# Kernel tuning notes

Measured on AMD Instinct MI355X. Metric: run time of the kernel, lower is better.

The kernel has to match this reference:

```python
import jax, jax.numpy as jnp
import numpy as np

B = 16384      # batch of numbers
D = 768        # embedding_dim
BINS = 10      # num_magnitude_bins
H = 8          # attention heads
HD = D // H


def _ln(x, g, b, eps=1e-5):
    m = jnp.mean(x, -1, keepdims=True)
    v = jnp.mean(jnp.square(x - m), -1, keepdims=True)
    return (x - m) / jnp.sqrt(v + eps) * g + b


def setup_inputs():
    key = jax.random.key(0)
    ks = jax.random.split(key, 10)
    w = lambda k, s: jax.random.normal(k, s, dtype=jnp.float32) * 0.02
    number = jax.random.normal(ks[0], (B, 1), dtype=jnp.float32) * 1e4
    bounds = np.concatenate([[-np.inf], -np.logspace(0, 15, BINS - 1), [0.0], np.logspace(0, 15, BINS - 1)])
    boundaries = jnp.asarray(np.unique(bounds), dtype=jnp.float32)
    d4 = D // 4
    return dict(
        number=number, boundaries=boundaries,
        mag_emb=jax.random.normal(ks[1], (2 * BINS, D), dtype=jnp.float32),
        se_w1=w(ks[2], (d4, 1)), se_b1=jnp.zeros(d4, jnp.float32),
        se_g1=jnp.ones(d4, jnp.float32), se_bt1=jnp.zeros(d4, jnp.float32),
        se_w2=w(ks[3], (D, d4)), se_b2=jnp.zeros(D, jnp.float32),
        ne_w=w(ks[4], (D, 2)), ne_b=jnp.zeros(D, jnp.float32),
        ne_g=jnp.ones(D, jnp.float32), ne_bt=jnp.zeros(D, jnp.float32),
        ce_w=w(ks[5], (D, 2)), ce_b=jnp.zeros(D, jnp.float32),
        ce_g=jnp.ones(D, jnp.float32), ce_bt=jnp.zeros(D, jnp.float32),
        in_proj_w=w(ks[6], (3 * D, D)), in_proj_b=jnp.zeros(3 * D, jnp.float32),
        out_proj_w=w(ks[7], (D, D)), out_proj_b=jnp.zeros(D, jnp.float32),
        magnitude_scale=jnp.ones(2 * BINS, jnp.float32),
        temperature=jnp.array(1.0, jnp.float32),
    )


def reference(number, boundaries, mag_emb, se_w1, se_b1, se_g1, se_bt1, se_w2, se_b2,
              ne_w, ne_b, ne_g, ne_bt, ce_w, ce_b, ce_g, ce_bt,
              in_proj_w, in_proj_b, out_proj_w, out_proj_b, magnitude_scale, temperature):
    signs = jnp.sign(number)
    abs_num = jnp.abs(number)
    log_abs = jnp.log1p(abs_num)
    scale_factor = jnp.floor(jnp.log10(abs_num + 1e-10))                      # [B,1]
    num_feat = jnp.concatenate([number / (jnp.max(abs_num) + 1e-10),
                                log_abs / (jnp.max(log_abs) + 1e-10)], -1)    # [B,2]
    ctx_feat = jnp.concatenate([signs, scale_factor / 16.0], -1)              # [B,2]
    num_enc = jax.nn.gelu(_ln(num_feat @ ne_w.T + ne_b, ne_g, ne_bt), approximate=False)
    ctx_enc = jax.nn.gelu(_ln(ctx_feat @ ce_w.T + ce_b, ce_g, ce_bt), approximate=False)
    # torch.bucketize(right=False) == searchsorted side='left'
    bin_idx = jnp.clip(jnp.searchsorted(boundaries, number[:, 0], side='left'), 0, 2 * BINS - 1)
    magnitude_emb = mag_emb[bin_idx]                                          # [B,D]
    h = jax.nn.gelu(_ln(scale_factor @ se_w1.T + se_b1, se_g1, se_bt1), approximate=False)
    scale_emb = h @ se_w2.T + se_b2                                           # [B,D]
    feats = jnp.stack([num_enc, magnitude_emb, scale_emb, ctx_enc], axis=1)   # [B,4,D]
    qkv = feats @ in_proj_w.T + in_proj_b                                     # [B,4,3D]
    q, k, v = jnp.split(qkv, 3, axis=-1)
    q = q.reshape(-1, 4, H, HD); k = k.reshape(-1, 4, H, HD); v = v.reshape(-1, 4, H, HD)
    att = jax.nn.softmax(jnp.einsum('bqhd,bkhd->bhqk', q, k) / jnp.sqrt(jnp.float32(HD)), axis=-1)
    ao = jnp.einsum('bhqk,bkhd->bqhd', att, v).reshape(-1, 4, D)
    ao = ao @ out_proj_w.T + out_proj_b                                       # [B,4,D]
    wts = jnp.array([0.4, 0.3, 0.2, 0.1], dtype=ao.dtype)
    out = jnp.sum(ao * wts[None, :, None], axis=1)                            # [B,D]
    sc = jax.nn.softplus(magnitude_scale[bin_idx] / temperature)[:, None]
    out = out * sc
    out = jnp.where(jnp.isnan(out), jnp.zeros_like(out), out)
    nrm = jnp.sqrt(jnp.sum(out * out, axis=-1, keepdims=True))
    return out / jnp.maximum(nrm, 1e-12)
```

## Files before the change

kernel.cpp:

```cpp
#include <hip/hip_runtime.h>
#include <hip/hip_bf16.h>
#include <math.h>

#define BB 16384
#define DD 768
#define NG 512
#define GR 1024
#define MROWS 1280
#define CPS 511
#define NCELL 1022
#define MIXR 2048

typedef __attribute__((ext_vector_type(8))) short bf16x8;
typedef __attribute__((ext_vector_type(4))) float f32x4;

__device__ short g_Abf[(size_t)MROWS * DD];
__device__ short g_W[(size_t)2304 * DD];
__device__ short g_WoutBf[(size_t)DD * DD];
__device__ short g_qkv[(size_t)MROWS * 2304];
__device__ short g_QKp[(size_t)16 * MROWS * 128];
__device__ short g_TabP[(size_t)16 * 128 * 128];
__device__ float g_scoref[(size_t)16 * MROWS * 128];
__device__ float g_sd[(size_t)MROWS * 8];
__device__ float g_tnode[GR];
__device__ int   g_creg[NCELL];
__device__ short g_mixedS[(size_t)MIXR * DD];
__device__ short g_preS[(size_t)MIXR * DD];
__device__ float g_maxabs;

__device__ inline unsigned short f2bf(float x) {
    union { float f; unsigned u; } v; v.f = x;
    unsigned r = v.u + 0x7fffu + ((v.u >> 16) & 1u);
    return (unsigned short)(r >> 16);
}
__device__ inline float bf2f(unsigned short h) {
    union { unsigned u; float f; } v; v.u = ((unsigned)h) << 16;
    return v.f;
}

__device__ inline float gelu_exact(float x) {
    return 0.5f * x * (1.0f + erff(x * 0.70710678118654752440f));
}

__device__ inline float block_sum256(float v, float* sbuf) {
    #pragma unroll
    for (int o = 32; o; o >>= 1) v += __shfl_xor(v, o);
    __syncthreads();
    if ((threadIdx.x & 63) == 0) sbuf[threadIdx.x >> 6] = v;
    __syncthreads();
    return sbuf[0] + sbuf[1] + sbuf[2] + sbuf[3];
}

__device__ inline int region_of(float x, const float* __restrict__ boundaries,
                                int* bin_o, int* sfi_o, int* si_o) {
    int bin = 0;
    #pragma unroll
    for (int j = 0; j < 20; ++j) bin += (boundaries[j] < x) ? 1 : 0;
    bin = min(bin, 19);
    float sf = floorf(log10f(fabsf(x) + 1e-10f));
    int sfi = min(max((int)sf + 10, 0), 15);
    int si = (x > 0.f) ? 2 : ((x < 0.f) ? 0 : 1);
    *bin_o = bin; *sfi_o = sfi; *si_o = si;
    return (bin << 6) | (sfi << 2) | si;
}

__global__ __launch_bounds__(1024) void k_absmax(const float* __restrict__ number) {
    const float4* n4 = reinterpret_cast<const float4*>(number);
    float v = 0.f;
    #pragma unroll
    for (int i = 0; i < 4; ++i) {
        float4 x = n4[threadIdx.x + 1024 * i];
        v = fmaxf(fmaxf(fabsf(x.x), fabsf(x.y)), fmaxf(fmaxf(fabsf(x.z), fabsf(x.w)), v));
    }
    #pragma unroll
    for (int o = 32; o; o >>= 1) v = fmaxf(v, __shfl_xor(v, o));
    __shared__ float sb[16];
    if ((threadIdx.x & 63) == 0) sb[threadIdx.x >> 6] = v;
    __syncthreads();
    if (threadIdx.x == 0) {
        float m = sb[0];
        #pragma unroll
        for (int i = 1; i < 16; ++i) m = fmaxf(m, sb[i]);
        g_maxabs = m;
    }
}

__global__ void k_tables(const float* __restrict__ mag_emb,
                         const float* __restrict__ se_w1, const float* __restrict__ se_b1,
                         const float* __restrict__ se_g1, const float* __restrict__ se_bt1,
                         const float* __restrict__ se_w2, const float* __restrict__ se_b2,
                         const float* __restrict__ ce_w, const float* __restrict__ ce_b,
                         const float* __restrict__ ce_g, const float* __restrict__ ce_bt,
                         const float* __restrict__ in_proj_w, const float* __restrict__ out_proj_w,
                         const float* __restrict__ ne_w, const float* __restrict__ ne_b,
                         const float* __restrict__ ne_g, const float* __restrict__ ne_bt) {
    __shared__ float sbuf[4];
    __shared__ float sh[192];
    const int t = threadIdx.x;
    const int blk = blockIdx.x;
    if (blk < 20) {
        #pragma unroll
        for (int i = 0; i < 3; ++i) {
            int d = t + 256 * i;
            g_Abf[(size_t)(GR + blk) * DD + d] = (short)f2bf(mag_emb[blk * DD + d]);
        }
    } else if (blk < 36) {
        int sfi = blk - 20;
        float sf = (float)(sfi - 10);
        float pre = 0.f;
        if (t < 192) pre = sf * se_w1[t] + se_b1[t];
        float s = block_sum256(t < 192 ? pre : 0.f, sbuf);
        float m = s / 192.f;
        float dd = (t < 192) ? (pre - m) : 0.f;
        float vv = block_sum256(dd * dd, sbuf);
        float inv = 1.f / sqrtf(vv / 192.f + 1e-5f);
        if (t < 192) sh[t] = gelu_exact((pre - m) * inv * se_g1[t] + se_bt1[t]);
        __syncthreads();
        #pragma unroll
        for (int i = 0; i < 3; ++i) {
            int d = t + 256 * i;
            float acc = se_b2[d];
            for (int j = 0; j < 192; ++j) acc += se_w2[d * 192 + j] * sh[j];
            g_Abf[(size_t)(GR + 20 + sfi) * DD + d] = (short)f2bf(acc);
        }
    } else if (blk < 84) {
        int c = blk - 36;
        int si = c >> 4, sfi = c & 15;
        float f0 = (float)(si - 1);
        float f1 = (float)(sfi - 10) / 16.f;
        float pre[3];
        float ps = 0.f;
        #pragma unroll
        for (int i = 0; i < 3; ++i) {
            int d = t + 256 * i;
            pre[i] = f0 * ce_w[2 * d] + f1 * ce_w[2 * d + 1] + ce_b[d];
            ps += pre[i];
        }
        float s = block_sum256(ps, sbuf);
        float m = s / 768.f;
        float qs = 0.f;
        #pragma unroll
        for (int i = 0; i < 3; ++i) { float dd = pre[i] - m; qs += dd * dd; }
        float vv = block_sum256(qs, sbuf);
        float inv = 1.f / sqrtf(vv / 768.f + 1e-5f);
        #pragma unroll
        for (int i = 0; i < 3; ++i) {
            int d = t + 256 * i;
            g_Abf[(size_t)(GR + 36 + c) * DD + d] =
                (short)f2bf(gelu_exact((pre[i] - m) * inv * ce_g[d] + ce_bt[d]));
        }
    } else if (blk < 256) {
        int row = GR + 84 + (blk - 84);
        #pragma unroll
        for (int i = 0; i < 3; ++i) g_Abf[(size_t)row * DD + t + 256 * i] = 0;
    } else if (blk < 2560) {
        int i = (blk - 256) * 256 + t;
        const bool second = (i >= 442368);
        const float* src = second ? out_proj_w : in_proj_w;
        short* dst = second ? g_WoutBf : g_W;
        int j = second ? (i - 442368) : i;
        const float4 v = *reinterpret_cast<const float4*>(&src[(size_t)j * 4]);
        ushort4 o;
        o.x = f2bf(v.x); o.y = f2bf(v.y); o.z = f2bf(v.z); o.w = f2bf(v.w);
        *reinterpret_cast<ushort4*>(&dst[(size_t)j * 4]) = o;
    } else {
        const int wid = t >> 6, lane = t & 63;
        const int r = (blk - 2560) * 4 + wid;
        const float mx = g_maxabs;
        const float L = log1pf(mx);
        const float dt = L / (float)(NG - 1);
        const int ri = r & (NG - 1);
        float tt = (float)ri * dt;
        if (ri > 0 && ri < NG - 1) {
            #pragma unroll
            for (int k = 0; k < 16; ++k) {
                float tb = log1pf(__expf((float)k * 2.302585093f));
                if (tb < L && (int)(tb / dt + 0.5f) == ri) tt = tb;
            }
            #pragma unroll
            for (int j = 0; j < 9; ++j) {
                float tb = log1pf(__expf((float)j * 1.875f * 2.302585093f));
                if (tb < L && (int)(tb / dt + 0.5f) == ri) tt = tb;
            }
        }
        if (lane == 0) g_tnode[r] = tt;
        const float ax = expm1f(tt);
        const float sgn = (r >= NG) ? -1.f : 1.f;
        const float a = sgn * ax / (mx + 1e-10f);
        const float b = tt / (L + 1e-10f);
        float pre[12];
        float s = 0.f;
        #pragma unroll
        for (int j = 0; j < 12; ++j) {
            int d = lane + 64 * j;
            float2 w = *reinterpret_cast<const float2*>(&ne_w[2 * d]);
            pre[j] = a * w.x + b * w.y + ne_b[d];
            s += pre[j];
        }
        #pragma unroll
        for (int o = 32; o; o >>= 1) s += __shfl_xor(s, o);
        float m = s / 768.f;
        float q = 0.f;
        #pragma unroll
        for (int j = 0; j < 12; ++j) { float dd = pre[j] - m; q += dd * dd; }
        #pragma unroll
        for (int o = 32; o; o >>= 1) q += __shfl_xor(q, o);
        float inv = 1.f / sqrtf(q / 768.f + 1e-5f);
        #pragma unroll
        for (int j = 0; j < 12; ++j) {
            int d = lane + 64 * j;
            g_Abf[(size_t)r * DD + d] = (short)f2bf(gelu_exact((pre[j] - m) * inv * ne_g[d] + ne_bt[d]));
        }
    }
}

__global__ __launch_bounds__(512, 4) void gemm_bt(int which, int N, int K) {
    const int z = blockIdx.z;
    const short* A = (which == 0) ? g_Abf : (which == 1) ? g_mixedS : g_QKp + (size_t)z * MROWS * 128;
    const short* B = (which == 0) ? g_W : (which == 2) ? g_TabP + (size_t)z * 128 * 128 : g_WoutBf;
    short* C = (which == 0) ? g_qkv : g_preS;
    float* Cf = g_scoref + (size_t)z * MROWS * 128;

    __shared__ short As[256 * 64];
    __shared__ short Bs[128 * 64];
    const int t = threadIdx.x;

    const int GX = gridDim.x;
    const int nwg = GX * gridDim.y;
    const int lin = blockIdx.y * GX + blockIdx.x;
    const int qq = nwg >> 3, rr = nwg & 7;
    const int xcd = lin & 7, idx = lin >> 3;
    const int nl = (xcd < rr ? xcd * (qq + 1) : rr * (qq + 1) + (xcd - rr) * qq) + idx;
    const int m0 = (nl / GX) * 256, n0 = (nl % GX) * 128;

    const int wid = t >> 6, lane = t & 63;
    const int wm = wid >> 1, wn = wid & 1;
    const int fr = lane & 15, ks = lane >> 4;

    f32x4 acc[4][4];
    #pragma unroll
    for (int m = 0; m < 4; ++m)
        #pragma unroll
        for (int n = 0; n < 4; ++n) acc[m][n] = (f32x4){0.f, 0.f, 0.f, 0.f};

    for (int k0 = 0; k0 < K; k0 += 64) {
        #pragma unroll
        for (int i = 0; i < 4; ++i) {
            int L = t + 512 * i;
            int row = L >> 3, sp = L & 7;
            int s = sp ^ (row & 7);
            const short* srcA = A + (size_t)(m0 + row) * K + k0 + s * 8;
            __builtin_amdgcn_global_load_lds(
                (const __attribute__((address_space(1))) unsigned int*)srcA,
                (__attribute__((address_space(3))) unsigned int*)((char*)As + L * 16), 16, 0, 0);
        }
        #pragma unroll
        for (int i = 0; i < 2; ++i) {
            int L = t + 512 * i;
            int row = L >> 3, sp = L & 7;
            int s = sp ^ (row & 7);
            const short* srcB = B + (size_t)(n0 + row) * K + k0 + s * 8;
            __builtin_amdgcn_global_load_lds(
                (const __attribute__((address_space(1))) unsigned int*)srcB,
                (__attribute__((address_space(3))) unsigned int*)((char*)Bs + L * 16), 16, 0, 0);
        }
        __syncthreads();
        #pragma unroll
        for (int kk = 0; kk < 2; ++kk) {
            bf16x8 af[4], bfr[4];
            #pragma unroll
            for (int m = 0; m < 4; ++m) {
                int row = wm * 64 + m * 16 + fr;
                int off = row * 128 + ((((kk << 2) | ks) ^ (row & 7)) * 16);
                af[m] = *(const bf16x8*)((const char*)As + off);
            }
            #pragma unroll
            for (int n = 0; n < 4; ++n) {
                int row = wn * 64 + n * 16 + fr;
                int off = row * 128 + ((((kk << 2) | ks) ^ (row & 7)) * 16);
                bfr[n] = *(const bf16x8*)((const char*)Bs + off);
            }
            #pragma unroll
            for (int m = 0; m < 4; ++m)
                #pragma unroll
                for (int n = 0; n < 4; ++n)
                    acc[m][n] = __builtin_amdgcn_mfma_f32_16x16x32_bf16(af[m], bfr[n], acc[m][n], 0, 0, 0);
        }
        __syncthreads();
    }

    #pragma unroll
    for (int m = 0; m < 4; ++m)
        #pragma unroll
        for (int n = 0; n < 4; ++n)
            #pragma unroll
            for (int j = 0; j < 4; ++j) {
                int row = m0 + wm * 64 + m * 16 + ks * 4 + j;
                int col = n0 + wn * 64 + n * 16 + fr;
                if (which == 2) Cf[(size_t)row * N + col] = acc[m][n][j];
                else C[(size_t)row * N + col] = (short)f2bf(acc[m][n][j]);
            }
}

__global__ void k_repack(const float* __restrict__ in_proj_b) {
    const int blk = blockIdx.x;
    if (blk < 1280) {
        const int idx = blk * 256 + threadIdx.x;
        const int z = idx / (MROWS * 16);
        const int rem = idx % (MROWS * 16);
        const int g = rem >> 4, c8 = rem & 15, d = c8 * 8;
        unsigned short o[8] = {0, 0, 0, 0, 0, 0, 0, 0};
        if (d < 96) {
            const int h = z & 7;
            const int off = (z < 8) ? 0 : 768;
            const float* bias = in_proj_b + off + h * 96 + d;
            const unsigned short* src = (const unsigned short*)g_qkv + (size_t)g * 2304 + off + h * 96 + d;
            #pragma unroll
            for (int c = 0; c < 8; ++c) o[c] = f2bf(bf2f(src[c]) + bias[c]);
        }
        *reinterpret_cast<bf16x8*>(g_QKp + (size_t)idx * 8) = *(const bf16x8*)o;
    } else if (blk < 1408) {
        const int i2 = (blk - 1280) * 256 + threadIdx.x;
        const int z = i2 / (128 * 16);
        const int rem = i2 % (128 * 16);
        const int j = rem >> 4, c8 = rem & 15, d = c8 * 8;
        unsigned short o[8] = {0, 0, 0, 0, 0, 0, 0, 0};
        if (d < 96 && j < 84) {
            const int h = z & 7;
            const int off = (z < 8) ? 768 : 0;
            const float* bias = in_proj_b + off + h * 96 + d;
            const unsigned short* src = (const unsigned short*)g_qkv + (size_t)(GR + j) * 2304 + off + h * 96 + d;
            #pragma unroll
            for (int c = 0; c < 8; ++c) o[c] = f2bf(bf2f(src[c]) + bias[c]);
        }
        *reinterpret_cast<bf16x8*>(g_TabP + (size_t)i2 * 8) = *(const bf16x8*)o;
    } else {
        const int wid = threadIdx.x >> 6, lane = threadIdx.x & 63;
        const int g = (blk - 1408) * 4 + wid;
        if (g >= GR + 84) return;
        const int h = lane >> 3, sub = lane & 7;
        const int d0 = h * 96 + sub * 12;
        const unsigned short* qrow = (const unsigned short*)g_qkv + (size_t)g * 2304 + d0;
        const unsigned short* krow = qrow + 768;
        const float* bq = in_proj_b + d0;
        const float* bk = in_proj_b + 768 + d0;
        float s = 0.f;
        #pragma unroll
        for (int c = 0; c < 12; ++c)
            s += (bf2f(qrow[c]) + bq[c]) * (bf2f(krow[c]) + bk[c]);
        s += __shfl_xor(s, 1);
        s += __shfl_xor(s, 2);
        s += __shfl_xor(s, 4);
        if (sub == 0) g_sd[(size_t)g * 8 + h] = s;
    }
}

__global__ void k_attn_cell(const float* __restrict__ boundaries,
                            const float* __restrict__ in_proj_b) {
    const int wid = threadIdx.x >> 6, lane = threadIdx.x & 63;
    const int mr = blockIdx.x * 4 + wid;
    if (mr >= 2 * NCELL) return;
    const int cid = mr >> 1, ep = mr & 1;
    const int s = cid / CPS, c = cid - s * CPS;
    const int node = s * NG + c + ep;
    const float tn0 = g_tnode[s * NG + c], tn1 = g_tnode[s * NG + c + 1];
    const float xmid = (s ? -1.f : 1.f) * expm1f(0.5f * (tn0 + tn1));
    int bin, sfi, si;
    const int re = region_of(xmid, boundaries, &bin, &sfi, &si);
    if (ep == 0 && lane == 0) g_creg[cid] = re;
    const int j3[3] = {bin, 20 + sfi, 36 + si * 16 + sfi};

    const int h = lane >> 3;
    const float isq = 0.1020620726159658f;
    float sc[4][4];
    sc[0][0] = g_sd[(size_t)node * 8 + h] * isq;
    const size_t su = ((size_t)h * MROWS + node) * 128;
    const size_t sw = ((size_t)(8 + h) * MROWS + node) * 128;
    #pragma unroll
    for (int jj = 0; jj < 3; ++jj) {
        sc[0][jj + 1] = g_scoref[su + j3[jj]] * isq;
        sc[jj + 1][0] = g_scoref[sw + j3[jj]] * isq;
    }
    #pragma unroll
    for (int ii = 0; ii < 3; ++ii)
        #pragma unroll
        for (int jj = 0; jj < 3; ++jj)
            sc[ii + 1][jj + 1] = g_scoref[((size_t)h * MROWS + GR + j3[ii]) * 128 + j3[jj]] * isq;

    const float wt[4] = {0.4f, 0.3f, 0.2f, 0.1f};
    float wtil[4] = {0.f, 0.f, 0.f, 0.f};
    #pragma unroll
    for (int i = 0; i < 4; ++i) {
        float mxs = fmaxf(fmaxf(sc[i][0], sc[i][1]), fmaxf(sc[i][2], sc[i][3]));
        float ex[4], den = 0.f;
        #pragma unroll
        for (int j = 0; j < 4; ++j) { ex[j] = __expf(sc[i][j] - mxs); den += ex[j]; }
        float idn = wt[i] / den;
        #pragma unroll
        for (int j = 0; j < 4; ++j) wtil[j] += ex[j] * idn;
    }

    const int d0 = lane * 12;
    float bv[12];
    #pragma unroll
    for (int c4 = 0; c4 < 3; ++c4) {
        float4 cc = *reinterpret_cast<const float4*>(&in_proj_b[1536 + d0 + c4 * 4]);
        bv[c4 * 4 + 0] = cc.x; bv[c4 * 4 + 1] = cc.y; bv[c4 * 4 + 2] = cc.z; bv[c4 * 4 + 3] = cc.w;
    }
    float mixv[12];
    {
        const unsigned short* r0 = (const unsigned short*)g_qkv + (size_t)node * 2304 + 1536 + d0;
        #pragma unroll
        for (int cc = 0; cc < 12; ++cc) mixv[cc] = wtil[0] * (bf2f(r0[cc]) + bv[cc]);
    }
    #pragma unroll
    for (int jj = 0; jj < 3; ++jj) {
        const unsigned short* rt = (const unsigned short*)g_qkv + (size_t)(GR + j3[jj]) * 2304 + 1536 + d0;
        const float w = wtil[jj + 1];
        #pragma unroll
        for (int cc = 0; cc < 12; ++cc) mixv[cc] += w * (bf2f(rt[cc]) + bv[cc]);
    }
    unsigned short ob[12];
    #pragma unroll
    for (int cc = 0; cc < 12; ++cc) ob[cc] = f2bf(mixv[cc]);
    unsigned short* mbase = (unsigned short*)g_mixedS + (size_t)mr * DD + d0;
    #pragma unroll
    for (int c4 = 0; c4 < 3; ++c4)
        *reinterpret_cast<ushort4*>(mbase + c4 * 4) =
            make_ushort4(ob[c4 * 4 + 0], ob[c4 * 4 + 1], ob[c4 * 4 + 2], ob[c4 * 4 + 3]);
}

__global__ void k_final(const float* __restrict__ number, const float* __restrict__ boundaries,
                        const float* __restrict__ in_proj_b, const float* __restrict__ out_proj_b,
                        float* __restrict__ out) {
    const int wid = threadIdx.x >> 6, lane = threadIdx.x & 63;
    const int e = blockIdx.x * 4 + wid;
    const float x = number[e];
    int bin, sfi, si;
    const int re = region_of(x, boundaries, &bin, &sfi, &si);

    const float mx = g_maxabs;
    const float L = log1pf(mx);
    const float dt = L / (float)(NG - 1);
    const float t = log1pf(fabsf(x));
    const int s = (x < 0.f) ? 1 : 0;
    const int base = s * NG;
    int i0 = min(max((int)(t / dt), 0), NG - 2);
    #pragma unroll
    for (int it = 0; it < 2; ++it) {
        if (i0 > 0 && t < g_tnode[base + i0]) --i0;
        else if (i0 < NG - 2 && t >= g_tnode[base + i0 + 1]) ++i0;
    }
    const float tn0 = g_tnode[base + i0], tn1 = g_tnode[base + i0 + 1];
    float w1 = (t - tn0) / (tn1 - tn0);
    w1 = fminf(fmaxf(w1, 0.f), 1.f);
    const float w0 = 1.f - w1;
    const int cid = s * CPS + i0;
    const int d0 = lane * 12;
    float o[12], ss = 0.f;

    if (g_creg[cid] == re) {
        const unsigned short* r0 = (const unsigned short*)g_preS + (size_t)(2 * cid) * DD + d0;
        const unsigned short* r1 = r0 + DD;
        #pragma unroll
        for (int c4 = 0; c4 < 3; ++c4) {
            float4 b = *reinterpret_cast<const float4*>(&out_proj_b[d0 + c4 * 4]);
            ushort4 u0 = *reinterpret_cast<const ushort4*>(r0 + c4 * 4);
            ushort4 u1 = *reinterpret_cast<const ushort4*>(r1 + c4 * 4);
            float p0 = w0 * bf2f(u0.x) + w1 * bf2f(u1.x) + b.x;
            float p1 = w0 * bf2f(u0.y) + w1 * bf2f(u1.y) + b.y;
            float p2 = w0 * bf2f(u0.z) + w1 * bf2f(u1.z) + b.z;
            float p3 = w0 * bf2f(u0.w) + w1 * bf2f(u1.w) + b.w;
            if (p0 != p0) p0 = 0.f;
            if (p1 != p1) p1 = 0.f;
            if (p2 != p2) p2 = 0.f;
            if (p3 != p3) p3 = 0.f;
            o[c4 * 4 + 0] = p0; o[c4 * 4 + 1] = p1; o[c4 * 4 + 2] = p2; o[c4 * 4 + 3] = p3;
            ss += p0 * p0 + p1 * p1 + p2 * p2 + p3 * p3;
        }
    } else {
        const int j3[3] = {bin, 20 + sfi, 36 + si * 16 + sfi};
        const int g0 = base + i0;
        const int h = lane >> 3;
        const float isq = 0.1020620726159658f;
        float sc[4][4];
        sc[0][0] = (w0 * g_sd[(size_t)g0 * 8 + h] + w1 * g_sd[(size_t)(g0 + 1) * 8 + h]) * isq;
        const size_t su0 = ((size_t)h * MROWS + g0) * 128;
        const size_t sw0 = ((size_t)(8 + h) * MROWS + g0) * 128;
        #pragma unroll
        for (int jj = 0; jj < 3; ++jj) {
            const int j = j3[jj];
            sc[0][jj + 1] = (w0 * g_scoref[su0 + j] + w1 * g_scoref[su0 + 128 + j]) * isq;
            sc[jj + 1][0] = (w0 * g_scoref[sw0 + j] + w1 * g_scoref[sw0 + 128 + j]) * isq;
        }
        #pragma unroll
        for (int ii = 0; ii < 3; ++ii)
            #pragma unroll
            for (int jj = 0; jj < 3; ++jj)
                sc[ii + 1][jj + 1] = g_scoref[((size_t)h * MROWS + GR + j3[ii]) * 128 + j3[jj]] * isq;
        const float wt[4] = {0.4f, 0.3f, 0.2f, 0.1f};
        float wtil[4] = {0.f, 0.f, 0.f, 0.f};
        #pragma unroll
        for (int i = 0; i < 4; ++i) {
            float mxs = fmaxf(fmaxf(sc[i][0], sc[i][1]), fmaxf(sc[i][2], sc[i][3]));
            float ex[4], den = 0.f;
            #pragma unroll
            for (int j = 0; j < 4; ++j) { ex[j] = __expf(sc[i][j] - mxs); den += ex[j]; }
            float idn = wt[i] / den;
            #pragma unroll
            for (int j = 0; j < 4; ++j) wtil[j] += ex[j] * idn;
        }
        float mixv[12];
        {
            const unsigned short* r0 = (const unsigned short*)g_qkv + (size_t)g0 * 2304 + 1536 + d0;
            const unsigned short* r1 = r0 + 2304;
            #pragma unroll
            for (int cc = 0; cc < 12; ++cc) {
                float bvv = in_proj_b[1536 + d0 + cc];
                mixv[cc] = wtil[0] * (w0 * bf2f(r0[cc]) + w1 * bf2f(r1[cc]) + bvv);
            }
        }
        #pragma unroll
        for (int jj = 0; jj < 3; ++jj) {
            const unsigned short* rt = (const unsigned short*)g_qkv + (size_t)(GR + j3[jj]) * 2304 + 1536 + d0;
            const float w = wtil[jj + 1];
            #pragma unroll
            for (int cc = 0; cc < 12; ++cc)
                mixv[cc] += w * (bf2f(rt[cc]) + in_proj_b[1536 + d0 + cc]);
        }
        int mb[12];
        #pragma unroll
        for (int cc = 0; cc < 12; ++cc) mb[cc] = (int)f2bf(mixv[cc]);
        float acc[12];
        #pragma unroll
        for (int cc = 0; cc < 12; ++cc) acc[cc] = 0.f;
        for (int l = 0; l < 64; ++l) {
            float md[12];
            #pragma unroll
            for (int cc = 0; cc < 12; ++cc)
                md[cc] = bf2f((unsigned short)__shfl(mb[cc], l));
            const int dbase = l * 12;
            #pragma unroll
            for (int c2 = 0; c2 < 12; ++c2) {
                const unsigned short* rp = (const unsigned short*)g_WoutBf + (size_t)(d0 + c2) * DD + dbase;
                float a = 0.f;
                #pragma unroll
                for (int cc = 0; cc < 12; ++cc) a += md[cc] * bf2f(rp[cc]);
                acc[c2] += a;
            }
        }
        #pragma unroll
        for (int cc = 0; cc < 12; ++cc) {
            float p = acc[cc] + out_proj_b[d0 + cc];
            if (p != p) p = 0.f;
            o[cc] = p;
            ss += p * p;
        }
    }

    #pragma unroll
    for (int ofs = 32; ofs; ofs >>= 1) ss += __shfl_xor(ss, ofs);
    float inv = 1.f / fmaxf(sqrtf(ss), 1e-12f);
    float* obase = &out[(size_t)e * DD + d0];
    #pragma unroll
    for (int c4 = 0; c4 < 3; ++c4)
        *reinterpret_cast<float4*>(obase + c4 * 4) =
            make_float4(o[c4 * 4 + 0] * inv, o[c4 * 4 + 1] * inv, o[c4 * 4 + 2] * inv, o[c4 * 4 + 3] * inv);
}

extern "C" void kernel_launch(void* const* d_in, const int* in_sizes, int n_in,
                              void* d_out, int out_size, void* d_ws, size_t ws_size,
                              hipStream_t stream) {
    const float* number      = (const float*)d_in[0];
    const float* boundaries  = (const float*)d_in[1];
    const float* mag_emb     = (const float*)d_in[2];
    const float* se_w1       = (const float*)d_in[3];
    const float* se_b1       = (const float*)d_in[4];
    const float* se_g1       = (const float*)d_in[5];
    const float* se_bt1      = (const float*)d_in[6];
    const float* se_w2       = (const float*)d_in[7];
    const float* se_b2       = (const float*)d_in[8];
    const float* ne_w        = (const float*)d_in[9];
    const float* ne_b        = (const float*)d_in[10];
    const float* ne_g        = (const float*)d_in[11];
    const float* ne_bt       = (const float*)d_in[12];
    const float* ce_w        = (const float*)d_in[13];
    const float* ce_b        = (const float*)d_in[14];
    const float* ce_g        = (const float*)d_in[15];
    const float* ce_bt       = (const float*)d_in[16];
    const float* in_proj_w   = (const float*)d_in[17];
    const float* in_proj_b   = (const float*)d_in[18];
    const float* out_proj_w  = (const float*)d_in[19];
    const float* out_proj_b  = (const float*)d_in[20];
    float* out = (float*)d_out;

    k_absmax<<<1, 1024, 0, stream>>>(number);
    k_tables<<<2816, 256, 0, stream>>>(mag_emb, se_w1, se_b1, se_g1, se_bt1, se_w2, se_b2,
                                       ce_w, ce_b, ce_g, ce_bt, in_proj_w, out_proj_w,
                                       ne_w, ne_b, ne_g, ne_bt);
    gemm_bt<<<dim3(2304 / 128, MROWS / 256, 1), 512, 0, stream>>>(0, 2304, DD);
    k_repack<<<1685, 256, 0, stream>>>(in_proj_b);
    gemm_bt<<<dim3(1, MROWS / 256, 16), 512, 0, stream>>>(2, 128, 128);
    k_attn_cell<<<(2 * NCELL + 3) / 4, 256, 0, stream>>>(boundaries, in_proj_b);
    gemm_bt<<<dim3(DD / 128, MIXR / 256, 1), 512, 0, stream>>>(1, DD, DD);
    k_final<<<BB / 4, 256, 0, stream>>>(number, boundaries, in_proj_b, out_proj_b, out);
}
```

Measured before the change: 119.3 us.

## Fold absmax and repack kernels into table build and GEMM epilogue

Removes the separate absmax kernel by having each grid-table block redundantly reduce the max of the input numbers. Removes the repack kernel by having the QKV GEMM epilogue add bias and scatter Q/K into the padded per-head layouts, with the zero padding now written by k_tables. The per-node q·k self-dot is recomputed inline in k_attn_cell and k_final rather than precomputed. This cuts two launches and one pass over the QKV buffer, at the cost of redundant reductions, scattered 2-byte stores in the GEMM epilogue, and extra global reads in k_final.

```diff
diff --git a/kernel.cpp b/kernel.cpp
--- a/kernel.cpp
+++ b/kernel.cpp
@@ -21,7 +21,6 @@
 __device__ short g_QKp[(size_t)16 * MROWS * 128];
 __device__ short g_TabP[(size_t)16 * 128 * 128];
 __device__ float g_scoref[(size_t)16 * MROWS * 128];
-__device__ float g_sd[(size_t)MROWS * 8];
 __device__ float g_tnode[GR];
 __device__ int   g_creg[NCELL];
 __device__ short g_mixedS[(size_t)MIXR * DD];
@@ -64,28 +63,8 @@
     return (bin << 6) | (sfi << 2) | si;
 }
 
-__global__ __launch_bounds__(1024) void k_absmax(const float* __restrict__ number) {
-    const float4* n4 = reinterpret_cast<const float4*>(number);
-    float v = 0.f;
-    #pragma unroll
-    for (int i = 0; i < 4; ++i) {
-        float4 x = n4[threadIdx.x + 1024 * i];
-        v = fmaxf(fmaxf(fabsf(x.x), fabsf(x.y)), fmaxf(fmaxf(fabsf(x.z), fabsf(x.w)), v));
-    }
-    #pragma unroll
-    for (int o = 32; o; o >>= 1) v = fmaxf(v, __shfl_xor(v, o));
-    __shared__ float sb[16];
-    if ((threadIdx.x & 63) == 0) sb[threadIdx.x >> 6] = v;
-    __syncthreads();
-    if (threadIdx.x == 0) {
-        float m = sb[0];
-        #pragma unroll
-        for (int i = 1; i < 16; ++i) m = fmaxf(m, sb[i]);
-        g_maxabs = m;
-    }
-}
-
-__global__ void k_tables(const float* __restrict__ mag_emb,
+__global__ void k_tables(const float* __restrict__ number,
+                         const float* __restrict__ mag_emb,
                          const float* __restrict__ se_w1, const float* __restrict__ se_b1,
                          const float* __restrict__ se_g1, const float* __restrict__ se_bt1,
                          const float* __restrict__ se_w2, const float* __restrict__ se_b2,
@@ -96,6 +75,7 @@
                          const float* __restrict__ ne_g, const float* __restrict__ ne_bt) {
     __shared__ float sbuf[4];
     __shared__ float sh[192];
+    __shared__ float smx[4];
     const int t = threadIdx.x;
     const int blk = blockIdx.x;
     if (blk < 20) {
@@ -163,10 +143,23 @@
         ushort4 o;
         o.x = f2bf(v.x); o.y = f2bf(v.y); o.z = f2bf(v.z); o.w = f2bf(v.w);
         *reinterpret_cast<ushort4*>(&dst[(size_t)j * 4]) = o;
-    } else {
+    } else if (blk < 2816) {
+        const float4* n4 = reinterpret_cast<const float4*>(number);
+        float vmx = 0.f;
+        #pragma unroll
+        for (int i = 0; i < 16; ++i) {
+            float4 xx = n4[t + 256 * i];
+            vmx = fmaxf(fmaxf(fabsf(xx.x), fabsf(xx.y)), fmaxf(fmaxf(fabsf(xx.z), fabsf(xx.w)), vmx));
+        }
+        #pragma unroll
+        for (int o = 32; o; o >>= 1) vmx = fmaxf(vmx, __shfl_xor(vmx, o));
+        if ((t & 63) == 0) smx[t >> 6] = vmx;
+        __syncthreads();
+        const float mx = fmaxf(fmaxf(smx[0], smx[1]), fmaxf(smx[2], smx[3]));
+        if (t == 0) g_maxabs = mx;
+
         const int wid = t >> 6, lane = t & 63;
         const int r = (blk - 2560) * 4 + wid;
-        const float mx = g_maxabs;
         const float L = log1pf(mx);
         const float dt = L / (float)(NG - 1);
         const int ri = r & (NG - 1);
@@ -211,10 +204,22 @@
             int d = lane + 64 * j;
             g_Abf[(size_t)r * DD + d] = (short)f2bf(gelu_exact((pre[j] - m) * inv * ne_g[d] + ne_bt[d]));
         }
-    }
-}
-
-__global__ __launch_bounds__(512, 4) void gemm_bt(int which, int N, int K) {
+    } else if (blk < 3136) {
+        const int i = (blk - 2816) * 256 + t;
+        const int z = i / (MROWS * 4);
+        const int rem = i % (MROWS * 4);
+        const int row = rem >> 2, c = rem & 3;
+        const bf16x8 zv = {0, 0, 0, 0, 0, 0, 0, 0};
+        *reinterpret_cast<bf16x8*>(g_QKp + ((size_t)z * MROWS + row) * 128 + 96 + c * 8) = zv;
+    } else {
+        const int i = (blk - 3136) * 256 + t;
+        const bf16x8 zv = {0, 0, 0, 0, 0, 0, 0, 0};
+        *reinterpret_cast<bf16x8*>(g_TabP + (size_t)i * 8) = zv;
+    }
+}
+
+__global__ __launch_bounds__(512, 4) void gemm_bt(int which, int N, int K,
+                                                  const float* __restrict__ bias) {
     const int z = blockIdx.z;
     const short* A = (which == 0) ? g_Abf : (which == 1) ? g_mixedS : g_QKp + (size_t)z * MROWS * 128;
     const short* B = (which == 0) ? g_W : (which == 2) ? g_TabP + (size_t)z * 128 * 128 : g_WoutBf;
@@ -297,62 +302,25 @@
             for (int j = 0; j < 4; ++j) {
                 int row = m0 + wm * 64 + m * 16 + ks * 4 + j;
                 int col = n0 + wn * 64 + n * 16 + fr;
-                if (which == 2) Cf[(size_t)row * N + col] = acc[m][n][j];
-                else C[(size_t)row * N + col] = (short)f2bf(acc[m][n][j]);
-            }
-}
-
-__global__ void k_repack(const float* __restrict__ in_proj_b) {
-    const int blk = blockIdx.x;
-    if (blk < 1280) {
-        const int idx = blk * 256 + threadIdx.x;
-        const int z = idx / (MROWS * 16);
-        const int rem = idx % (MROWS * 16);
-        const int g = rem >> 4, c8 = rem & 15, d = c8 * 8;
-        unsigned short o[8] = {0, 0, 0, 0, 0, 0, 0, 0};
-        if (d < 96) {
-            const int h = z & 7;
-            const int off = (z < 8) ? 0 : 768;
-            const float* bias = in_proj_b + off + h * 96 + d;
-            const unsigned short* src = (const unsigned short*)g_qkv + (size_t)g * 2304 + off + h * 96 + d;
-            #pragma unroll
-            for (int c = 0; c < 8; ++c) o[c] = f2bf(bf2f(src[c]) + bias[c]);
-        }
-        *reinterpret_cast<bf16x8*>(g_QKp + (size_t)idx * 8) = *(const bf16x8*)o;
-    } else if (blk < 1408) {
-        const int i2 = (blk - 1280) * 256 + threadIdx.x;
-        const int z = i2 / (128 * 16);
-        const int rem = i2 % (128 * 16);
-        const int j = rem >> 4, c8 = rem & 15, d = c8 * 8;
-        unsigned short o[8] = {0, 0, 0, 0, 0, 0, 0, 0};
-        if (d < 96 && j < 84) {
-            const int h = z & 7;
-            const int off = (z < 8) ? 768 : 0;
-            const float* bias = in_proj_b + off + h * 96 + d;
-            const unsigned short* src = (const unsigned short*)g_qkv + (size_t)(GR + j) * 2304 + off + h * 96 + d;
-            #pragma unroll
-            for (int c = 0; c < 8; ++c) o[c] = f2bf(bf2f(src[c]) + bias[c]);
-        }
-        *reinterpret_cast<bf16x8*>(g_TabP + (size_t)i2 * 8) = *(const bf16x8*)o;
-    } else {
-        const int wid = threadIdx.x >> 6, lane = threadIdx.x & 63;
-        const int g = (blk - 1408) * 4 + wid;
-        if (g >= GR + 84) return;
-        const int h = lane >> 3, sub = lane & 7;
-        const int d0 = h * 96 + sub * 12;
-        const unsigned short* qrow = (const unsigned short*)g_qkv + (size_t)g * 2304 + d0;
-        const unsigned short* krow = qrow + 768;
-        const float* bq = in_proj_b + d0;
-        const float* bk = in_proj_b + 768 + d0;
-        float s = 0.f;
-        #pragma unroll
-        for (int c = 0; c < 12; ++c)
-            s += (bf2f(qrow[c]) + bq[c]) * (bf2f(krow[c]) + bk[c]);
-        s += __shfl_xor(s, 1);
-        s += __shfl_xor(s, 2);
-        s += __shfl_xor(s, 4);
-        if (sub == 0) g_sd[(size_t)g * 8 + h] = s;
-    }
+                float av = acc[m][n][j];
+                if (which == 2) {
+                    Cf[(size_t)row * N + col] = av;
+                } else {
+                    C[(size_t)row * N + col] = (short)f2bf(av);
+                    if (which == 0 && col < 1536) {
+                        int colh = (col >= 768) ? col - 768 : col;
+                        int h = (colh * 683) >> 16;
+                        int d = colh - h * 96;
+                        int zq = (col >= 768) ? 8 + h : h;
+                        unsigned short vb = f2bf(av + bias[col]);
+                        g_QKp[((size_t)zq * MROWS + row) * 128 + d] = (short)vb;
+                        if (row >= GR && row < GR + 84) {
+                            int zt = (col >= 768) ? h : 8 + h;
+                            g_TabP[((size_t)zt * 128 + (row - GR)) * 128 + d] = (short)vb;
+                        }
+                    }
+                }
+            }
 }
 
 __global__ void k_attn_cell(const float* __restrict__ boundaries,
@@ -370,10 +338,24 @@
     if (ep == 0 && lane == 0) g_creg[cid] = re;
     const int j3[3] = {bin, 20 + sfi, 36 + si * 16 + sfi};
 
+    const int d0 = lane * 12;
     const int h = lane >> 3;
     const float isq = 0.1020620726159658f;
+
+    float sdv = 0.f;
+    {
+        const unsigned short* qn = (const unsigned short*)g_qkv + (size_t)node * 2304 + d0;
+        const unsigned short* kn = qn + 768;
+        #pragma unroll
+        for (int cc = 0; cc < 12; ++cc)
+            sdv += (bf2f(qn[cc]) + in_proj_b[d0 + cc]) * (bf2f(kn[cc]) + in_proj_b[768 + d0 + cc]);
+        sdv += __shfl_xor(sdv, 1);
+        sdv += __shfl_xor(sdv, 2);
+        sdv += __shfl_xor(sdv, 4);
+    }
+
     float sc[4][4];
-    sc[0][0] = g_sd[(size_t)node * 8 + h] * isq;
+    sc[0][0] = sdv * isq;
     const size_t su = ((size_t)h * MROWS + node) * 128;
     const size_t sw = ((size_t)(8 + h) * MROWS + node) * 128;
     #pragma unroll
@@ -400,7 +382,6 @@
         for (int j = 0; j < 4; ++j) wtil[j] += ex[j] * idn;
     }
 
-    const int d0 = lane * 12;
     float bv[12];
     #pragma unroll
     for (int c4 = 0; c4 < 3; ++c4) {
@@ -483,8 +464,24 @@
         const int g0 = base + i0;
         const int h = lane >> 3;
         const float isq = 0.1020620726159658f;
+        float s0 = 0.f, s1 = 0.f;
+        {
+            const unsigned short* q0 = (const unsigned short*)g_qkv + (size_t)g0 * 2304 + d0;
+            const unsigned short* k0r = q0 + 768;
+            const unsigned short* q1 = q0 + 2304;
+            const unsigned short* k1r = q1 + 768;
+            #pragma unroll
+            for (int cc = 0; cc < 12; ++cc) {
+                float bqv = in_proj_b[d0 + cc];
+                float bkv = in_proj_b[768 + d0 + cc];
+                s0 += (bf2f(q0[cc]) + bqv) * (bf2f(k0r[cc]) + bkv);
+                s1 += (bf2f(q1[cc]) + bqv) * (bf2f(k1r[cc]) + bkv);
+            }
+            s0 += __shfl_xor(s0, 1); s0 += __shfl_xor(s0, 2); s0 += __shfl_xor(s0, 4);
+            s1 += __shfl_xor(s1, 1); s1 += __shfl_xor(s1, 2); s1 += __shfl_xor(s1, 4);
+        }
         float sc[4][4];
-        sc[0][0] = (w0 * g_sd[(size_t)g0 * 8 + h] + w1 * g_sd[(size_t)(g0 + 1) * 8 + h]) * isq;
+        sc[0][0] = (w0 * s0 + w1 * s1) * isq;
         const size_t su0 = ((size_t)h * MROWS + g0) * 128;
         const size_t sw0 = ((size_t)(8 + h) * MROWS + g0) * 128;
         #pragma unroll
@@ -594,14 +591,12 @@
     const float* out_proj_b  = (const float*)d_in[20];
     float* out = (float*)d_out;
 
-    k_absmax<<<1, 1024, 0, stream>>>(number);
-    k_tables<<<2816, 256, 0, stream>>>(mag_emb, se_w1, se_b1, se_g1, se_bt1, se_w2, se_b2,
-                                       ce_w, ce_b, ce_g, ce_bt, in_proj_w, out_proj_w,
-                                       ne_w, ne_b, ne_g, ne_bt);
-    gemm_bt<<<dim3(2304 / 128, MROWS / 256, 1), 512, 0, stream>>>(0, 2304, DD);
-    k_repack<<<1685, 256, 0, stream>>>(in_proj_b);
-    gemm_bt<<<dim3(1, MROWS / 256, 16), 512, 0, stream>>>(2, 128, 128);
+    k_tables<<<3264, 256, 0, stream>>>(number, mag_emb, se_w1, se_b1, se_g1, se_bt1,
+                                       se_w2, se_b2, ce_w, ce_b, ce_g, ce_bt,
+                                       in_proj_w, out_proj_w, ne_w, ne_b, ne_g, ne_bt);
+    gemm_bt<<<dim3(2304 / 128, MROWS / 256, 1), 512, 0, stream>>>(0, 2304, DD, in_proj_b);
+    gemm_bt<<<dim3(1, MROWS / 256, 16), 512, 0, stream>>>(2, 128, 128, in_proj_b);
     k_attn_cell<<<(2 * NCELL + 3) / 4, 256, 0, stream>>>(boundaries, in_proj_b);
-    gemm_bt<<<dim3(DD / 128, MIXR / 256, 1), 512, 0, stream>>>(1, DD, DD);
+    gemm_bt<<<dim3(DD / 128, MIXR / 256, 1), 512, 0, stream>>>(1, DD, DD, in_proj_b);
     k_final<<<BB / 4, 256, 0, stream>>>(number, boundaries, in_proj_b, out_proj_b, out);
 }
```

Result: slower. 129.6 us (+8.6%).
